# Kernel tuning notes

Measured on AMD Instinct MI355X. Metric: run time of the kernel, lower is better.

The kernel has to match this reference:

```python
import jax, jax.numpy as jnp
import numpy as np

B, T_TGT, T_SRC, H, V = 4, 256, 512, 1024, 32100


def setup_inputs() -> dict:
    key = jax.random.key(0)
    ks = jax.random.split(key, 7)
    return {
        "decoder_hidden_states": jax.random.normal(ks[0], (B, T_TGT, H), dtype=jnp.float32),
        "cross_attention_weights": jax.random.uniform(ks[1], (B, T_TGT, T_SRC), dtype=jnp.float32),
        "encoder_hidden_states": jax.random.normal(ks[2], (B, T_SRC, H), dtype=jnp.float32),
        "vocab_logits": jax.random.normal(ks[3], (B, T_TGT, V), dtype=jnp.float32),
        "W_gen": jax.random.normal(ks[4], (2 * H, 1), dtype=jnp.float32) * (1.0 / np.sqrt(2 * H)),
        "b_gen": jnp.zeros((1,), dtype=jnp.float32),
        "source_ids": jax.random.randint(ks[5], (B, T_SRC), 0, V, dtype=jnp.int64).astype(jnp.int32),
        "vocab_size": V,
    }


def reference(decoder_hidden_states, cross_attention_weights, encoder_hidden_states,
              vocab_logits, W_gen, b_gen, source_ids, vocab_size):
    # context vector: (B, T_tgt, H) = attn (B,T_tgt,T_src) @ enc (B,T_src,H)
    context = jnp.einsum('bts,bsh->bth', cross_attention_weights, encoder_hidden_states)
    gen_input = jnp.concatenate([context, decoder_hidden_states], axis=-1)  # (B,T_tgt,2H)
    p_gen = jax.nn.sigmoid(gen_input @ W_gen + b_gen)  # (B,T_tgt,1)

    vocab_dist = jax.nn.softmax(vocab_logits, axis=-1)  # (B,T_tgt,V)

    # scatter-add attention mass onto vocab ids; duplicates accumulate
    def scatter_one(ids, attn):  # ids (T_src,), attn (T_tgt,T_src)
        return jnp.zeros((attn.shape[0], vocab_size), attn.dtype).at[:, ids].add(attn)

    copy_dist = jax.vmap(scatter_one)(source_ids, cross_attention_weights)  # (B,T_tgt,V)

    final_dist = p_gen * vocab_dist + (1.0 - p_gen) * copy_dist + 1e-12
    return jnp.log(final_dist)
```

## Files before the change

### kernel.cpp

```cpp
#include <hip/hip_runtime.h>
#include <hip/hip_bf16.h>
#include <math.h>
#include <string.h>

#define NB 4
#define TT 256
#define TS 512
#define HH 1024
#define VV 32100
#define V4 8025
#define NT 1024
#define KREG 8
#define ROWS 4
#define HASHN 1024

typedef float nfloat4 __attribute__((ext_vector_type(4)));

__global__ __launch_bounds__(256) void precompute_dots(
    const float* __restrict__ dec, const float* __restrict__ enc,
    const float* __restrict__ Wg, const float* __restrict__ bg,
    float* __restrict__ e, float* __restrict__ g2)
{
    int row  = blockIdx.x * 4 + (threadIdx.x >> 6);
    int lane = threadIdx.x & 63;

    const float4* s4;
    const float4* w4;
    float bias = 0.0f;
    float* dst;

    if (row < NB * TS) {
        s4  = (const float4*)(enc + (size_t)row * HH);
        w4  = (const float4*)Wg;
        dst = e + row;
    } else {
        int rr = row - NB * TS;
        if (rr >= NB * TT) return;
        s4   = (const float4*)(dec + (size_t)rr * HH);
        w4   = (const float4*)(Wg + HH);
        bias = bg[0];
        dst  = g2 + rr;
    }

    float acc = 0.0f;
#pragma unroll
    for (int i = lane; i < HH / 4; i += 64) {
        float4 a = s4[i];
        float4 w = w4[i];
        acc += a.x * w.x + a.y * w.y + a.z * w.z + a.w * w.w;
    }
#pragma unroll
    for (int off = 32; off >= 1; off >>= 1)
        acc += __shfl_xor(acc, off);
    if (lane == 0) *dst = acc + bias;
}

__device__ __forceinline__ unsigned pack2(float a, float b) {
    __hip_bfloat162 h = __float22bfloat162_rn(make_float2(a, b));
    unsigned u; memcpy(&u, &h, 4); return u;
}
__device__ __forceinline__ float unpk_lo(unsigned u) {
    unsigned x = u << 16; float f; memcpy(&f, &x, 4); return f;
}
__device__ __forceinline__ float unpk_hi(unsigned u) {
    unsigned x = u & 0xffff0000u; float f; memcpy(&f, &x, 4); return f;
}
__device__ __forceinline__ void nt_store4(float4 o, float4* addr) {
    nfloat4 n = { o.x, o.y, o.z, o.w };
    __builtin_nontemporal_store(n, (nfloat4*)addr);
}

__global__ __launch_bounds__(NT, 4) void pg_fused(
    const float* __restrict__ attn, const int* __restrict__ ids,
    const float* __restrict__ logits, const float* __restrict__ e,
    const float* __restrict__ g2, float* __restrict__ out)
{
    __shared__ int   hkey[ROWS][HASHN];
    __shared__ float hval[ROWS][HASHN];
    __shared__ float redz[16], redd[16], redn[16];
    __shared__ float bcst[ROWS][4];

    const int tid  = threadIdx.x;
    const int blk  = blockIdx.x;
    const int r0   = blk * ROWS;
    const int b    = r0 >> 8;
    const int wid  = tid >> 6;
    const int lane = tid & 63;

    float4   v[KREG];
    unsigned pA[2 * KREG], pB[2 * KREG];
    float    s = 0.0f, part = 0.0f, lmin = 3.4e38f, av = 0.0f;
    int      idv = 0;

#define LOADR(r) {                                                            \
    const float4* lp = (const float4*)(logits + (size_t)(r) * VV);            \
    _Pragma("unroll")                                                         \
    for (int k = 0; k < KREG; ++k) {                                          \
        int f  = tid + NT * k;                                                \
        int fc = (k < KREG - 1) ? f : ((f < V4) ? f : (V4 - 1));              \
        v[k] = lp[fc];                                                        \
    } }

#define HASHR(i, r) {                                                         \
    if (tid < TS) {                                                           \
        av   = attn[(size_t)(r) * TS + tid];                                  \
        idv  = ids[b * TS + tid];                                             \
        part = av * e[b * TS + tid];                                          \
        unsigned slot = (((unsigned)idv * 0x9E3779B1u) >> 22) & (HASHN - 1);  \
        while (true) {                                                        \
            int prev = atomicCAS(&hkey[i][slot], -1, idv);                    \
            if (prev == -1 || prev == idv) {                                  \
                atomicAdd(&hval[i][slot], av); break;                         \
            }                                                                 \
            slot = (slot + 1) & (HASHN - 1);                                  \
        }                                                                     \
    } else part = 0.0f; }

#define PROCR(pp) {                                                           \
    s = 0.0f; lmin = 3.4e38f;                                                 \
    _Pragma("unroll")                                                         \
    for (int k = 0; k < KREG; ++k) {                                          \
        float4 w  = v[k];                                                     \
        float add = __expf(w.x) + __expf(w.y) + __expf(w.z) + __expf(w.w);    \
        float mn  = fminf(fminf(w.x, w.y), fminf(w.z, w.w));                  \
        if (k == KREG - 1 && tid + NT * k >= V4) { add = 0.0f; mn = 3.4e38f; }\
        s += add; lmin = fminf(lmin, mn);                                     \
        pp[2 * k]     = pack2(w.x, w.y);                                      \
        pp[2 * k + 1] = pack2(w.z, w.w);                                      \
    }                                                                         \
    _Pragma("unroll")                                                         \
    for (int k = 0; k < 2 * KREG; ++k) asm volatile("" : "+v"(pp[k])); }

#define REDR(i, r) {                                                          \
    _Pragma("unroll")                                                         \
    for (int off = 32; off >= 1; off >>= 1) {                                 \
        s    += __shfl_xor(s, off);                                           \
        part += __shfl_xor(part, off);                                        \
        lmin  = fminf(lmin, __shfl_xor(lmin, off));                           \
    }                                                                         \
    if (lane == 0) { redz[wid] = s; redd[wid] = part; redn[wid] = lmin; }     \
    __syncthreads();                                                          \
    if (tid == 0) {                                                           \
        float Z = 0.0f, d = 0.0f, mn = 3.4e38f;                               \
        _Pragma("unroll")                                                     \
        for (int w2 = 0; w2 < 16; ++w2) {                                     \
            Z += redz[w2]; d += redd[w2]; mn = fminf(mn, redn[w2]);           \
        }                                                                     \
        float pg  = 1.0f / (1.0f + __expf(-(d + g2[r])));                     \
        float pzv = pg / Z;                                                   \
        bcst[i][0] = pzv;                                                     \
        bcst[i][1] = 1.0f - pg;                                               \
        bcst[i][2] = __logf(pzv);                                             \
        bcst[i][3] = (pzv * __expf(mn) >= 1e-10f) ? 1.0f : 0.0f;              \
    }                                                                         \
    __syncthreads(); }

#define WRITER(i, r, pp) {                                                    \
    float4* op = (float4*)(out + (size_t)(r) * VV);                           \
    const float pzv  = bcst[i][0];                                            \
    const float lpz  = bcst[i][2];                                            \
    const bool  fstr = bcst[i][3] > 0.5f;                                     \
    if (fstr) {                                                               \
        _Pragma("unroll")                                                     \
        for (int k = 0; k < KREG; ++k) {                                      \
            int f = tid + NT * k;                                             \
            if (k == KREG - 1 && f >= V4) continue;                           \
            float4 o;                                                         \
            o.x = unpk_lo(pp[2 * k])     + lpz;                               \
            o.y = unpk_hi(pp[2 * k])     + lpz;                               \
            o.z = unpk_lo(pp[2 * k + 1]) + lpz;                               \
            o.w = unpk_hi(pp[2 * k + 1]) + lpz;                               \
            nt_store4(o, &op[f]);                                             \
        }                                                                     \
    } else {                                                                  \
        _Pragma("unroll")                                                     \
        for (int k = 0; k < KREG; ++k) {                                      \
            int f = tid + NT * k;                                             \
            if (k == KREG - 1 && f >= V4) continue;                           \
            float4 o;                                                         \
            o.x = __logf(fmaf(pzv, __expf(unpk_lo(p p## _dummy                \
            )), 1e-12f));                                                     \
        }                                                                     \
    } }

#undef WRITER
#define WRITER(i, r, pp) {                                                    \
    float4* op = (float4*)(out + (size_t)(r) * VV);                           \
    const float pzv  = bcst[i][0];                                            \
    const float lpz  = bcst[i][2];                                            \
    const bool  fstr = bcst[i][3] > 0.5f;                                     \
    _Pragma("unroll")                                                         \
    for (int k = 0; k < KREG; ++k) {                                          \
        int f = tid + NT * k;                                                 \
        if (k == KREG - 1 && f >= V4) continue;                               \
        float4 o;                                                             \
        if (fstr) {                                                           \
            o.x = unpk_lo(pp[2 * k])     + lpz;                               \
            o.y = unpk_hi(pp[2 * k])     + lpz;                               \
            o.z = unpk_lo(pp[2 * k + 1]) + lpz;                               \
            o.w = unpk_hi(pp[2 * k + 1]) + lpz;                               \
        } else {                                                              \
            o.x = __logf(fmaf(pzv, __expf(unpk_lo(pp[2 * k])),     1e-12f));  \
            o.y = __logf(fmaf(pzv, __expf(unpk_hi(pp[2 * k])),     1e-12f));  \
            o.z = __logf(fmaf(pzv, __expf(unpk_lo(pp[2 * k + 1])), 1e-12f));  \
            o.w = __logf(fmaf(pzv, __expf(unpk_hi(pp[2 * k + 1])), 1e-12f));  \
        }                                                                     \
        nt_store4(o, &op[f]);                                                 \
    } }

#define FIXR(i, r) {                                                          \
    int key = hkey[i][tid];                                                   \
    if (key >= 0) {                                                           \
        float c   = hval[i][tid];                                             \
        float pzv = bcst[i][0], qv = bcst[i][1];                              \
        float l   = logits[(size_t)(r) * VV + key];                           \
        out[(size_t)(r) * VV + key] =                                         \
            __logf(fmaf(pzv, __expf(l), fmaf(qv, c, 1e-12f)));                \
    } }

#pragma unroll
    for (int i = 0; i < ROWS; ++i) { hkey[i][tid] = -1; hval[i][tid] = 0.0f; }
    __syncthreads();

    LOADR(r0); HASHR(0, r0); PROCR(pA);

    REDR(0, r0);
    LOADR(r0 + 1); WRITER(0, r0, pA); HASHR(1, r0 + 1); PROCR(pB);
    __syncthreads(); FIXR(0, r0);

    REDR(1, r0 + 1);
    LOADR(r0 + 2); WRITER(1, r0 + 1, pB); HASHR(2, r0 + 2); PROCR(pA);
    __syncthreads(); FIXR(1, r0 + 1);

    REDR(2, r0 + 2);
    LOADR(r0 + 3); WRITER(2, r0 + 2, pA); HASHR(3, r0 + 3); PROCR(pB);
    __syncthreads(); FIXR(2, r0 + 2);

    REDR(3, r0 + 3);
    WRITER(3, r0 + 3, pB);
    __syncthreads(); FIXR(3, r0 + 3);

#undef LOADR
#undef HASHR
#undef PROCR
#undef REDR
#undef WRITER
#undef FIXR
}

extern "C" void kernel_launch(void* const* d_in, const int* in_sizes, int n_in,
                              void* d_out, int out_size, void* d_ws, size_t ws_size,
                              hipStream_t stream) {
    const float* dec    = (const float*)d_in[0];
    const float* attn   = (const float*)d_in[1];
    const float* enc    = (const float*)d_in[2];
    const float* logits = (const float*)d_in[3];
    const float* Wg     = (const float*)d_in[4];
    const float* bg     = (const float*)d_in[5];
    const int*   ids    = (const int*)d_in[6];
    float* out = (float*)d_out;

    float* e  = (float*)d_ws;
    float* g2 = e + NB * TS;

    precompute_dots<<<(NB * TS + NB * TT) / 4, 256, 0, stream>>>(
        dec, enc, Wg, bg, e, g2);

    pg_fused<<<NB * TT / ROWS, NT, 0, stream>>>(attn, ids, logits, e, g2, out);
}
```

Baseline: 65.52 us.

## Stage packed bf16 logits rows in LDS and double-buffer hash tables

The packed bf16 copy of each logits row now lives in a two-slot shared-memory buffer instead of two per-thread register arrays, and the per-row hash tables shrink from four slots to two, cleared in FIXR and reused. The row pipeline is reordered so that the write of one row overlaps the processing and hashing of the next. The aim is to free many VGPRs and simplify the pipeline. In exchange, shared memory per block grows to roughly 140KB, which likely allows only one 1024-thread block per CU and adds LDS traffic on both the write and read side.

After: 65.85 us. Within noise of the previous version (+0.5%).

```diff
diff --git a/kernel.cpp b/kernel.cpp
--- a/kernel.cpp
+++ b/kernel.cpp
@@ -75,22 +75,21 @@
     const float* __restrict__ logits, const float* __restrict__ e,
     const float* __restrict__ g2, float* __restrict__ out)
 {
-    __shared__ int   hkey[ROWS][HASHN];
-    __shared__ float hval[ROWS][HASHN];
+    __shared__ uint2 lbuf[2][V4 + 3];
+    __shared__ int   hkey[2][HASHN];
+    __shared__ float hval[2][HASHN];
     __shared__ float redz[16], redd[16], redn[16];
-    __shared__ float bcst[ROWS][4];
+    __shared__ float bc[2][4];
 
     const int tid  = threadIdx.x;
-    const int blk  = blockIdx.x;
-    const int r0   = blk * ROWS;
+    const int r0   = blockIdx.x * ROWS;
     const int b    = r0 >> 8;
     const int wid  = tid >> 6;
     const int lane = tid & 63;
 
-    float4   v[KREG];
-    unsigned pA[2 * KREG], pB[2 * KREG];
-    float    s = 0.0f, part = 0.0f, lmin = 3.4e38f, av = 0.0f;
-    int      idv = 0;
+    float4 v[KREG];
+    float  s = 0.0f, part = 0.0f, lmin = 3.4e38f, av = 0.0f;
+    int    idv = 0;
 
 #define LOADR(r) {                                                            \
     const float4* lp = (const float4*)(logits + (size_t)(r) * VV);            \
@@ -99,39 +98,60 @@
         int f  = tid + NT * k;                                                \
         int fc = (k < KREG - 1) ? f : ((f < V4) ? f : (V4 - 1));              \
         v[k] = lp[fc];                                                        \
+    }                                                                         \
+    asm volatile("" ::: "memory");   }
+
+#define WRITER(bi, r) {                                                       \
+    float4* op = (float4*)(out + (size_t)(r) * VV);                           \
+    const float pzv  = bc[bi][0];                                             \
+    const float lpz  = bc[bi][2];                                             \
+    const bool  fstr = bc[bi][3] > 0.5f;                                      \
+    _Pragma("unroll")                                                         \
+    for (int k = 0; k < KREG; ++k) {                                          \
+        int f = tid + NT * k;                                                 \
+        if (k == KREG - 1 && f >= V4) continue;                               \
+        uint2 w = lbuf[bi][f];                                                \
+        float4 o;                                                             \
+        if (fstr) {                                                           \
+            o.x = unpk_lo(w.x) + lpz;  o.y = unpk_hi(w.x) + lpz;              \
+            o.z = unpk_lo(w.y) + lpz;  o.w = unpk_hi(w.y) + lpz;              \
+        } else {                                                              \
+            o.x = __logf(fmaf(pzv, __expf(unpk_lo(w.x)), 1e-12f));            \
+            o.y = __logf(fmaf(pzv, __expf(unpk_hi(w.x)), 1e-12f));            \
+            o.z = __logf(fmaf(pzv, __expf(unpk_lo(w.y)), 1e-12f));            \
+            o.w = __logf(fmaf(pzv, __expf(unpk_hi(w.y)), 1e-12f));            \
+        }                                                                     \
+        nt_store4(o, &op[f]);                                                 \
     } }
 
-#define HASHR(i, r) {                                                         \
+#define PROCR(bi) {                                                           \
+    s = 0.0f; lmin = 3.4e38f;                                                 \
+    _Pragma("unroll")                                                         \
+    for (int k = 0; k < KREG; ++k) {                                          \
+        int f = tid + NT * k;                                                 \
+        float4 w = v[k];                                                      \
+        if (k == KREG - 1 && f >= V4) continue;                               \
+        s    += __expf(w.x) + __expf(w.y) + __expf(w.z) + __expf(w.w);        \
+        lmin  = fminf(lmin, fminf(fminf(w.x, w.y), fminf(w.z, w.w)));         \
+        lbuf[bi][f] = make_uint2(pack2(w.x, w.y), pack2(w.z, w.w));           \
+    } }
+
+#define HASHR(bi, r) {                                                        \
     if (tid < TS) {                                                           \
         av   = attn[(size_t)(r) * TS + tid];                                  \
         idv  = ids[b * TS + tid];                                             \
         part = av * e[b * TS + tid];                                          \
         unsigned slot = (((unsigned)idv * 0x9E3779B1u) >> 22) & (HASHN - 1);  \
         while (true) {                                                        \
-            int prev = atomicCAS(&hkey[i][slot], -1, idv);                    \
+            int prev = atomicCAS(&hkey[bi][slot], -1, idv);                   \
             if (prev == -1 || prev == idv) {                                  \
-                atomicAdd(&hval[i][slot], av); break;                         \
+                atomicAdd(&hval[bi][slot], av); break;                        \
             }                                                                 \
             slot = (slot + 1) & (HASHN - 1);                                  \
         }                                                                     \
     } else part = 0.0f; }
 
-#define PROCR(pp) {                                                           \
-    s = 0.0f; lmin = 3.4e38f;                                                 \
-    _Pragma("unroll")                                                         \
-    for (int k = 0; k < KREG; ++k) {                                          \
-        float4 w  = v[k];                                                     \
-        float add = __expf(w.x) + __expf(w.y) + __expf(w.z) + __expf(w.w);    \
-        float mn  = fminf(fminf(w.x, w.y), fminf(w.z, w.w));                  \
-        if (k == KREG - 1 && tid + NT * k >= V4) { add = 0.0f; mn = 3.4e38f; }\
-        s += add; lmin = fminf(lmin, mn);                                     \
-        pp[2 * k]     = pack2(w.x, w.y);                                      \
-        pp[2 * k + 1] = pack2(w.z, w.w);                                      \
-    }                                                                         \
-    _Pragma("unroll")                                                         \
-    for (int k = 0; k < 2 * KREG; ++k) asm volatile("" : "+v"(pp[k])); }
-
-#define REDR(i, r) {                                                          \
+#define REDR(bi, r) {                                                         \
     _Pragma("unroll")                                                         \
     for (int off = 32; off >= 1; off >>= 1) {                                 \
         s    += __shfl_xor(s, off);                                           \
@@ -148,103 +168,66 @@
         }                                                                     \
         float pg  = 1.0f / (1.0f + __expf(-(d + g2[r])));                     \
         float pzv = pg / Z;                                                   \
-        bcst[i][0] = pzv;                                                     \
-        bcst[i][1] = 1.0f - pg;                                               \
-        bcst[i][2] = __logf(pzv);                                             \
-        bcst[i][3] = (pzv * __expf(mn) >= 1e-10f) ? 1.0f : 0.0f;              \
+        bc[bi][0] = pzv;                                                      \
+        bc[bi][1] = 1.0f - pg;                                                \
+        bc[bi][2] = __logf(pzv);                                              \
+        bc[bi][3] = (pzv * __expf(mn) >= 1e-10f) ? 1.0f : 0.0f;               \
     }                                                                         \
     __syncthreads(); }
 
-#define WRITER(i, r, pp) {                                                    \
-    float4* op = (float4*)(out + (size_t)(r) * VV);                           \
-    const float pzv  = bcst[i][0];                                            \
-    const float lpz  = bcst[i][2];                                            \
-    const bool  fstr = bcst[i][3] > 0.5f;                                     \
-    if (fstr) {                                                               \
-        _Pragma("unroll")                                                     \
-        for (int k = 0; k < KREG; ++k) {                                      \
-            int f = tid + NT * k;                                             \
-            if (k == KREG - 1 && f >= V4) continue;                           \
-            float4 o;                                                         \
-            o.x = unpk_lo(pp[2 * k])     + lpz;                               \
-            o.y = unpk_hi(pp[2 * k])     + lpz;                               \
-            o.z = unpk_lo(pp[2 * k + 1]) + lpz;                               \
-            o.w = unpk_hi(pp[2 * k + 1]) + lpz;                               \
-            nt_store4(o, &op[f]);                                             \
-        }                                                                     \
-    } else {                                                                  \
-        _Pragma("unroll")                                                     \
-        for (int k = 0; k < KREG; ++k) {                                      \
-            int f = tid + NT * k;                                             \
-            if (k == KREG - 1 && f >= V4) continue;                           \
-            float4 o;                                                         \
-            o.x = __logf(fmaf(pzv, __expf(unpk_lo(p p## _dummy                \
-            )), 1e-12f));                                                     \
-        }                                                                     \
-    } }
-
-#undef WRITER
-#define WRITER(i, r, pp) {                                                    \
-    float4* op = (float4*)(out + (size_t)(r) * VV);                           \
-    const float pzv  = bcst[i][0];                                            \
-    const float lpz  = bcst[i][2];                                            \
-    const bool  fstr = bcst[i][3] > 0.5f;                                     \
-    _Pragma("unroll")                                                         \
-    for (int k = 0; k < KREG; ++k) {                                          \
-        int f = tid + NT * k;                                                 \
-        if (k == KREG - 1 && f >= V4) continue;                               \
-        float4 o;                                                             \
-        if (fstr) {                                                           \
-            o.x = unpk_lo(pp[2 * k])     + lpz;                               \
-            o.y = unpk_hi(pp[2 * k])     + lpz;                               \
-            o.z = unpk_lo(pp[2 * k + 1]) + lpz;                               \
-            o.w = unpk_hi(pp[2 * k + 1]) + lpz;                               \
-        } else {                                                              \
-            o.x = __logf(fmaf(pzv, __expf(unpk_lo(pp[2 * k])),     1e-12f));  \
-            o.y = __logf(fmaf(pzv, __expf(unpk_hi(pp[2 * k])),     1e-12f));  \
-            o.z = __logf(fmaf(pzv, __expf(unpk_lo(pp[2 * k + 1])), 1e-12f));  \
-            o.w = __logf(fmaf(pzv, __expf(unpk_hi(pp[2 * k + 1])), 1e-12f));  \
-        }                                                                     \
-        nt_store4(o, &op[f]);                                                 \
-    } }
-
-#define FIXR(i, r) {                                                          \
-    int key = hkey[i][tid];                                                   \
+#define FIXR(bi, r) {                                                         \
+    int key = hkey[bi][tid];                                                  \
     if (key >= 0) {                                                           \
-        float c   = hval[i][tid];                                             \
-        float pzv = bcst[i][0], qv = bcst[i][1];                              \
+        float c   = hval[bi][tid];                                            \
+        float pzv = bc[bi][0], qv = bc[bi][1];                                \
         float l   = logits[(size_t)(r) * VV + key];                           \
         out[(size_t)(r) * VV + key] =                                         \
             __logf(fmaf(pzv, __expf(l), fmaf(qv, c, 1e-12f)));                \
+        hkey[bi][tid] = -1; hval[bi][tid] = 0.0f;            \
     } }
 
-#pragma unroll
-    for (int i = 0; i < ROWS; ++i) { hkey[i][tid] = -1; hval[i][tid] = 0.0f; }
-    __syncthreads();
-
-    LOADR(r0); HASHR(0, r0); PROCR(pA);
-
+    hkey[0][tid] = -1; hval[0][tid] = 0.0f;
+    hkey[1][tid] = -1; hval[1][tid] = 0.0f;
+    __syncthreads();
+
+    LOADR(r0);
+    HASHR(0, r0);
+    PROCR(0);
     REDR(0, r0);
-    LOADR(r0 + 1); WRITER(0, r0, pA); HASHR(1, r0 + 1); PROCR(pB);
-    __syncthreads(); FIXR(0, r0);
-
+
+    LOADR(r0 + 1);
+    WRITER(0, r0);
+    PROCR(1);
+    HASHR(1, r0 + 1);
     REDR(1, r0 + 1);
-    LOADR(r0 + 2); WRITER(1, r0 + 1, pB); HASHR(2, r0 + 2); PROCR(pA);
-    __syncthreads(); FIXR(1, r0 + 1);
-
-    REDR(2, r0 + 2);
-    LOADR(r0 + 3); WRITER(2, r0 + 2, pA); HASHR(3, r0 + 3); PROCR(pB);
-    __syncthreads(); FIXR(2, r0 + 2);
-
-    REDR(3, r0 + 3);
-    WRITER(3, r0 + 3, pB);
-    __syncthreads(); FIXR(3, r0 + 3);
+    FIXR(0, r0);
+    __syncthreads();
+
+    LOADR(r0 + 2);
+    WRITER(1, r0 + 1);
+    PROCR(0);
+    HASHR(0, r0 + 2);
+    REDR(0, r0 + 2);
+    FIXR(1, r0 + 1);
+    __syncthreads();
+
+    LOADR(r0 + 3);
+    WRITER(0, r0 + 2);
+    PROCR(1);
+    HASHR(1, r0 + 3);
+    REDR(1, r0 + 3);
+    FIXR(0, r0 + 2);
+    __syncthreads();
+
+    WRITER(1, r0 + 3);
+    __syncthreads();
+    FIXR(1, r0 + 3);
 
 #undef LOADR
+#undef WRITER
+#undef PROCR
 #undef HASHR
-#undef PROCR
 #undef REDR
-#undef WRITER
 #undef FIXR
 }
 
```
